# Kernel optimization log

Hardware: AMD Instinct MI355X
Metric: run time of the kernel (lower is better)

## Reference

```python
import jax, jax.numpy as jnp
import numpy as np

B, T, I, H, L, O = 512, 512, 64, 256, 3, 1  # batch, seq_len, input, hidden, layers, output


def setup_inputs() -> dict:
    key = jax.random.key(0)
    ks = jax.random.split(key, 16)
    s = 1.0 / np.sqrt(H)  # PyTorch nn.RNN init: U(-1/sqrt(H), 1/sqrt(H))
    u = lambda k, shape: jax.random.uniform(k, shape, jnp.float32, -s, s)
    inp = {"x": jax.random.normal(ks[0], (B, T, I), jnp.float32)}
    in_sizes = [I, H, H]
    for l in range(L):
        inp[f"w_ih{l}"] = u(ks[1 + 4 * l], (H, in_sizes[l]))
        inp[f"w_hh{l}"] = u(ks[2 + 4 * l], (H, H))
        inp[f"b_ih{l}"] = u(ks[3 + 4 * l], (H,))
        inp[f"b_hh{l}"] = u(ks[4 + 4 * l], (H,))
    inp["w_fc"] = u(ks[13], (O, H))
    inp["b_fc"] = u(ks[14], (O,))
    return inp


def _rnn_layer(x, w_ih, w_hh, b_ih, b_hh):
    # x: [B, T, in] -> outputs [B, T, H]; h_t = tanh(x_t W_ih^T + b_ih + h_{t-1} W_hh^T + b_hh)
    pre = jnp.einsum('bti,hi->bth', x, w_ih) + b_ih + b_hh  # input projection for all t at once

    def step(h, p_t):
        h = jnp.tanh(p_t + h @ w_hh.T)
        return h, h

    h0 = jnp.zeros((x.shape[0], w_hh.shape[0]), x.dtype)
    _, ys = jax.lax.scan(step, h0, pre.transpose(1, 0, 2))  # scan over time
    return ys.transpose(1, 0, 2)


def reference(x, w_ih0, w_hh0, b_ih0, b_hh0, w_ih1, w_hh1, b_ih1, b_hh1,
              w_ih2, w_hh2, b_ih2, b_hh2, w_fc, b_fc):
    h = _rnn_layer(x, w_ih0, w_hh0, b_ih0, b_hh0)
    h = _rnn_layer(h, w_ih1, w_hh1, b_ih1, b_hh1)
    h = _rnn_layer(h, w_ih2, w_hh2, b_ih2, b_hh2)
    out = h[:, -1, :] @ w_fc.T + b_fc  # [B, 1]
    return out.squeeze()  # [B]
```

## Files before the change

kernel.cpp:

```cpp
#include <hip/hip_runtime.h>
#include <cstdint>
#include <cstddef>

#define Tsz 512
#define TC  32
#define NCH 16

typedef _Float16 f16;
typedef _Float16 half8_t __attribute__((ext_vector_type(8)));
typedef _Float16 half4_t __attribute__((ext_vector_type(4)));
typedef float float4_t __attribute__((ext_vector_type(4)));

__device__ __forceinline__ float fast_exp2(float x) {
  float r; asm("v_exp_f32 %0, %1" : "=v"(r) : "v"(x)); return r;
}
__device__ __forceinline__ void pin(half8_t& v) { asm("" : "+v"(v)); }

#define BARRIER_LG asm volatile("s_waitcnt lgkmcnt(0)\n\ts_barrier" ::: "memory")

__device__ __forceinline__ size_t poff(int tile, int slot, int t, int j, int q) {
  return (((size_t)((tile * 2 + slot) * TC + t) * 256 + j) << 6) + ((size_t)q << 4);
}

template<int LAYER>
__device__ __forceinline__ void rec01_body(
    char* const smem, const int chunk, const int tile,
    const float* __restrict__ Pin, float* __restrict__ Pout,
    const f16* __restrict__ whh_h, const f16* __restrict__ wihn_h,
    const float* __restrict__ biasc, f16* __restrict__ st)
{
  char* const h_lds = smem;
  const int tid  = threadIdx.x;
  const int lane = tid & 63;
  const int wave = tid >> 6;
  const int m    = lane & 15;
  const int q    = lane >> 4;
  const int lo   = m * 16;
  const int slot = chunk & 1;
  const int j    = wave * 16 + m;

  half8_t whh[8], wihn[8];
  float biasn = biasc[(LAYER + 1) * 256 + j];
#pragma unroll
  for (int c = 0; c < 8; ++c) whh[c]  = *(const half8_t*)(whh_h  + j * 256 + c * 32 + q * 8);
#pragma unroll
  for (int c = 0; c < 8; ++c) wihn[c] = *(const half8_t*)(wihn_h + j * 256 + c * 32 + q * 8);
#pragma unroll
  for (int c = 0; c < 8; ++c) { pin(whh[c]); pin(wihn[c]); }

  if (tid < 512) {
    if (chunk == 0)
      *(float4_t*)(h_lds + tid * 16) = float4_t{0.f, 0.f, 0.f, 0.f};
    else
      *(float4_t*)(h_lds + tid * 16) = *(const float4_t*)((const char*)st + tile * 8192 + tid * 16);
  }

  float4_t pld[2];
  auto pload = [&](int tl, float4_t* d) {
    const int tn = (tl > TC - 1) ? (TC - 1) : tl;
    d[0] = *(const float4_t*)((const char*)Pin + poff(tile, slot, tn, j, q));
  };
  pload(0, &pld[0]); pload(1, &pld[1]);
  BARRIER_LG;

#pragma unroll 2
  for (int tl = 0; tl < TC; ++tl) {
    char* cur = h_lds + (tl & 1) * 8192;
    char* nxt = h_lds + ((tl + 1) & 1) * 8192;

    half8_t hf[4];
#pragma unroll
    for (int c = 0; c < 4; ++c) hf[c] = *(const half8_t*)(cur + (c * 4 + q) * 256 + lo);
    float4_t a0 = pld[tl & 1];
#pragma unroll
    for (int c = 0; c < 4; ++c)
      a0 = __builtin_amdgcn_mfma_f32_16x16x32_f16(hf[c], whh[c], a0, 0, 0, 0);
    float4_t b0 = {biasn, biasn, biasn, biasn};
    if (tl >= 1) {
#pragma unroll
      for (int c = 0; c < 4; ++c)
        b0 = __builtin_amdgcn_mfma_f32_16x16x32_f16(hf[c], wihn[c], b0, 0, 0, 0);
    }
#pragma unroll
    for (int c = 0; c < 4; ++c) hf[c] = *(const half8_t*)(cur + ((c + 4) * 4 + q) * 256 + lo);
    float4_t a1 = {0.f, 0.f, 0.f, 0.f};
#pragma unroll
    for (int c = 0; c < 4; ++c)
      a1 = __builtin_amdgcn_mfma_f32_16x16x32_f16(hf[c], whh[c + 4], a1, 0, 0, 0);
    if (tl >= 1) {
#pragma unroll
      for (int c = 0; c < 4; ++c)
        b0 = __builtin_amdgcn_mfma_f32_16x16x32_f16(hf[c], wihn[c + 4], b0, 0, 0, 0);
      *(float4_t*)((char*)Pout + poff(tile, slot, tl - 1, j, q)) = b0;
    }
    pload(tl + 2, &pld[tl & 1]);

    const float4_t acc = a0 + a1;
#pragma unroll
    for (int r = 0; r < 4; ++r) {
      const float e  = fast_exp2(acc[r] * 2.8853900817779268f);
      const float hv = 1.0f - 2.0f * __builtin_amdgcn_rcpf(1.0f + e);
      const int b = q * 4 + r;
      *(f16*)(nxt + (j >> 3) * 256 + b * 16 + (j & 7) * 2) = (f16)hv;
    }
    BARRIER_LG;
  }

  {
    half8_t hf[4];
    float4_t b0 = {biasn, biasn, biasn, biasn};
#pragma unroll
    for (int c = 0; c < 4; ++c) hf[c] = *(const half8_t*)(h_lds + (c * 4 + q) * 256 + lo);
#pragma unroll
    for (int c = 0; c < 4; ++c)
      b0 = __builtin_amdgcn_mfma_f32_16x16x32_f16(hf[c], wihn[c], b0, 0, 0, 0);
#pragma unroll
    for (int c = 0; c < 4; ++c) hf[c] = *(const half8_t*)(h_lds + ((c + 4) * 4 + q) * 256 + lo);
#pragma unroll
    for (int c = 0; c < 4; ++c)
      b0 = __builtin_amdgcn_mfma_f32_16x16x32_f16(hf[c], wihn[c + 4], b0, 0, 0, 0);
    *(float4_t*)((char*)Pout + poff(tile, slot, TC - 1, j, q)) = b0;
  }
  if (tid < 512)
    *(float4_t*)((char*)st + tile * 8192 + tid * 16) = *(const float4_t*)(h_lds + tid * 16);
}

template<bool REC, bool PRE>
__device__ __forceinline__ void l2_body(
    char* const smem, const int chunk, const int pre_chunk, const int tile,
    const f16* __restrict__ xh, const float* __restrict__ Pin, float* __restrict__ Pout,
    const f16* __restrict__ whh_h, const f16* __restrict__ wih0_h,
    const float* __restrict__ biasc, f16* __restrict__ st)
{
  char* const h_lds = smem;
  const int tid  = threadIdx.x;
  const int lane = tid & 63;
  const int wave = tid >> 6;
  const int m    = lane & 15;
  const int q    = lane >> 4;
  const int lo   = m * 16;
  const int slot  = chunk & 1;
  const int pslot = pre_chunk & 1;
  const int j    = wave * 16 + m;

  half8_t whh[8], wih0[2];
  float bias0 = 0.f;
  if constexpr (PRE) {
    bias0 = biasc[j];
#pragma unroll
    for (int c = 0; c < 2; ++c) wih0[c] = *(const half8_t*)(wih0_h + j * 64 + c * 32 + q * 8);
    pin(wih0[0]); pin(wih0[1]);
  }
  if constexpr (REC) {
#pragma unroll
    for (int c = 0; c < 8; ++c) whh[c] = *(const half8_t*)(whh_h + j * 256 + c * 32 + q * 8);
#pragma unroll
    for (int c = 0; c < 8; ++c) pin(whh[c]);
  }

  float4_t pld[2];
  auto pload = [&](int tl, float4_t* d) {
    const int tn = (tl > TC - 1) ? (TC - 1) : tl;
    d[0] = *(const float4_t*)((const char*)Pin + poff(tile, slot, tn, j, q));
  };
  half8_t xp[2][2];
  auto xload = [&](int tl, half8_t* d) {
    const int tn = (tl > TC - 1) ? (TC - 1) : tl;
    const f16* base = xh + ((size_t)(tile * 16 + m) * Tsz + (pre_chunk * TC + tn)) * 64 + q * 8;
    d[0] = *(const half8_t*)base;
    d[1] = *(const half8_t*)(base + 32);
  };

  if constexpr (REC) {
    if (tid < 512) {
      if (chunk == 0)
        *(float4_t*)(h_lds + tid * 16) = float4_t{0.f, 0.f, 0.f, 0.f};
      else
        *(float4_t*)(h_lds + tid * 16) = *(const float4_t*)((const char*)st + tile * 8192 + tid * 16);
    }
    pload(0, &pld[0]); pload(1, &pld[1]);
  }
  if constexpr (PRE) { xload(0, xp[0]); xload(1, xp[1]); }
  if constexpr (REC) BARRIER_LG;

#pragma unroll 2
  for (int tl = 0; tl < TC; ++tl) {
    if constexpr (REC) {
      char* cur = h_lds + (tl & 1) * 8192;
      char* nxt = h_lds + ((tl + 1) & 1) * 8192;
      half8_t hf[4];
#pragma unroll
      for (int c = 0; c < 4; ++c) hf[c] = *(const half8_t*)(cur + (c * 4 + q) * 256 + lo);
      float4_t a0 = pld[tl & 1];
#pragma unroll
      for (int c = 0; c < 4; ++c)
        a0 = __builtin_amdgcn_mfma_f32_16x16x32_f16(hf[c], whh[c], a0, 0, 0, 0);
#pragma unroll
      for (int c = 0; c < 4; ++c) hf[c] = *(const half8_t*)(cur + ((c + 4) * 4 + q) * 256 + lo);
      float4_t a1 = {0.f, 0.f, 0.f, 0.f};
#pragma unroll
      for (int c = 0; c < 4; ++c)
        a1 = __builtin_amdgcn_mfma_f32_16x16x32_f16(hf[c], whh[c + 4], a1, 0, 0, 0);
      pload(tl + 2, &pld[tl & 1]);
      const float4_t acc = a0 + a1;
#pragma unroll
      for (int r = 0; r < 4; ++r) {
        const float e  = fast_exp2(acc[r] * 2.8853900817779268f);
        const float hv = 1.0f - 2.0f * __builtin_amdgcn_rcpf(1.0f + e);
        const int b = q * 4 + r;
        *(f16*)(nxt + (j >> 3) * 256 + b * 16 + (j & 7) * 2) = (f16)hv;
      }
    }
    if constexpr (PRE) {
      float4_t b = {bias0, bias0, bias0, bias0};
      b = __builtin_amdgcn_mfma_f32_16x16x32_f16(xp[tl & 1][0], wih0[0], b, 0, 0, 0);
      b = __builtin_amdgcn_mfma_f32_16x16x32_f16(xp[tl & 1][1], wih0[1], b, 0, 0, 0);
      xload(tl + 2, xp[tl & 1]);
      *(float4_t*)((char*)Pout + poff(tile, pslot, tl, j, q)) = b;
    }
    if constexpr (REC) BARRIER_LG;
  }

  if constexpr (REC) {
    if (tid < 512)
      *(float4_t*)((char*)st + tile * 8192 + tid * 16) = *(const float4_t*)(h_lds + tid * 16);
  }
}

__global__ __launch_bounds__(1024)
void rnn_chunk_kernel(const f16* __restrict__ xh,
                      float* P0, float* P1, float* P2,
                      const f16* __restrict__ whh0h, const f16* __restrict__ whh1h,
                      const f16* __restrict__ whh2h, const f16* __restrict__ wih0h,
                      const f16* __restrict__ wih1h, const f16* __restrict__ wih2h,
                      const float* __restrict__ biasc,
                      f16* st0, f16* st1, f16* st2, int k)
{
  __shared__ __align__(16) char smem[16384];
  const int layer = blockIdx.x >> 5;
  const int tile  = blockIdx.x & 31;
  if (layer == 0) {
    if (k < NCH) rec01_body<0>(smem, k, tile, P0, P1, whh0h, wih1h, biasc, st0);
  } else if (layer == 1) {
    const int c = k - 1;
    if (c >= 0 && c < NCH) rec01_body<1>(smem, c, tile, P1, P2, whh1h, wih2h, biasc, st1);
  } else {
    const int c  = k - 2;
    const int pc = k + 1;
    const bool rec = (c >= 0 && c < NCH);
    const bool pre = (pc < NCH);
    if (rec && pre)  l2_body<true,  true >(smem, c, pc, tile, xh, P2, P0, whh2h, wih0h, biasc, st2);
    else if (rec)    l2_body<true,  false>(smem, c, pc, tile, xh, P2, P0, whh2h, wih0h, biasc, st2);
    else if (pre)    l2_body<false, true >(smem, c, pc, tile, xh, P2, P0, whh2h, wih0h, biasc, st2);
  }
}

__global__ __launch_bounds__(1024)
void pre0_kernel(const f16* __restrict__ xh, float* P0,
                 const f16* __restrict__ wih0h, const float* __restrict__ biasc)
{
  __shared__ __align__(16) char smem[16384];
  l2_body<false, true>(smem, 0, 0, blockIdx.x, xh, nullptr, P0, nullptr, wih0h, biasc, nullptr);
}

__global__ void prep_x_kernel(const float* __restrict__ x, f16* __restrict__ xh) {
  const size_t i = ((size_t)blockIdx.x * 256 + threadIdx.x) * 8;
  const float4_t v0 = *(const float4_t*)(x + i);
  const float4_t v1 = *(const float4_t*)(x + i + 4);
  half8_t o;
#pragma unroll
  for (int u = 0; u < 4; ++u) { o[u] = (f16)v0[u]; o[u + 4] = (f16)v1[u]; }
  *(half8_t*)(xh + i) = o;
}

__global__ void prep_kernel(const float* __restrict__ wih0, const float* __restrict__ whh0,
                            const float* __restrict__ bih0, const float* __restrict__ bhh0,
                            const float* __restrict__ wih1, const float* __restrict__ whh1,
                            const float* __restrict__ bih1, const float* __restrict__ bhh1,
                            const float* __restrict__ wih2, const float* __restrict__ whh2,
                            const float* __restrict__ bih2, const float* __restrict__ bhh2,
                            f16* wih0h, f16* whh0h, f16* wih1h, f16* whh1h,
                            f16* wih2h, f16* whh2h, float* biasc)
{
  const int i = blockIdx.x * 256 + threadIdx.x;
  if      (i < 16384)  wih0h[i]          = (f16)wih0[i];
  else if (i < 81920)  whh0h[i - 16384]  = (f16)whh0[i - 16384];
  else if (i < 147456) wih1h[i - 81920]  = (f16)wih1[i - 81920];
  else if (i < 212992) whh1h[i - 147456] = (f16)whh1[i - 147456];
  else if (i < 278528) wih2h[i - 212992] = (f16)wih2[i - 212992];
  else if (i < 344064) whh2h[i - 278528] = (f16)whh2[i - 278528];
  else if (i < 344320) biasc[i - 344064]       = bih0[i - 344064] + bhh0[i - 344064];
  else if (i < 344576) biasc[256 + i - 344320] = bih1[i - 344320] + bhh1[i - 344320];
  else if (i < 344832) biasc[512 + i - 344576] = bih2[i - 344576] + bhh2[i - 344576];
}

__global__ void fc_kernel(const f16* __restrict__ st2, const float* __restrict__ w_fc,
                          const float* __restrict__ b_fc, float* __restrict__ outp) {
  const int b = blockIdx.x;
  const int lane = threadIdx.x;
  const int tile = b >> 4, bl = b & 15;
  const int j = lane * 4;
  const char* hp = (const char*)st2 + tile * 8192 + (j >> 3) * 256 + bl * 16 + (j & 7) * 2;
  const half4_t hv = *(const half4_t*)hp;
  const float4_t w = *(const float4_t*)(w_fc + j);
  float s = (float)hv[0] * w[0] + (float)hv[1] * w[1] + (float)hv[2] * w[2] + (float)hv[3] * w[3];
#pragma unroll
  for (int off = 32; off > 0; off >>= 1) s += __shfl_down(s, off, 64);
  if (lane == 0) outp[b] = s + b_fc[0];
}

extern "C" void kernel_launch(void* const* d_in, const int* in_sizes, int n_in,
                              void* d_out, int out_size, void* d_ws, size_t ws_size,
                              hipStream_t stream) {
  const float* x     = (const float*)d_in[0];
  const float* w_ih0 = (const float*)d_in[1];
  const float* w_hh0 = (const float*)d_in[2];
  const float* b_ih0 = (const float*)d_in[3];
  const float* b_hh0 = (const float*)d_in[4];
  const float* w_ih1 = (const float*)d_in[5];
  const float* w_hh1 = (const float*)d_in[6];
  const float* b_ih1 = (const float*)d_in[7];
  const float* b_hh1 = (const float*)d_in[8];
  const float* w_ih2 = (const float*)d_in[9];
  const float* w_hh2 = (const float*)d_in[10];
  const float* b_ih2 = (const float*)d_in[11];
  const float* b_hh2 = (const float*)d_in[12];
  const float* w_fc  = (const float*)d_in[13];
  const float* b_fc  = (const float*)d_in[14];

  char* ws = (char*)d_ws;
  float* P0   = (float*)(ws);
  float* P1   = (float*)(ws + 33554432);
  float* P2   = (float*)(ws + 67108864);
  f16* st0    = (f16*)(ws + 100663296);
  f16* st1    = (f16*)(ws + 100925440);
  f16* st2    = (f16*)(ws + 101187584);
  f16* wih0h  = (f16*)(ws + 101449728);
  f16* whh0h  = (f16*)(ws + 101482496);
  f16* wih1h  = (f16*)(ws + 101613568);
  f16* whh1h  = (f16*)(ws + 101744640);
  f16* wih2h  = (f16*)(ws + 101875712);
  f16* whh2h  = (f16*)(ws + 102006784);
  float* biasc = (float*)(ws + 102137856);
  f16* xh     = (f16*)(ws + 102141952);

  prep_x_kernel<<<8192, 256, 0, stream>>>(x, xh);
  prep_kernel<<<1347, 256, 0, stream>>>(w_ih0, w_hh0, b_ih0, b_hh0,
                                        w_ih1, w_hh1, b_ih1, b_hh1,
                                        w_ih2, w_hh2, b_ih2, b_hh2,
                                        wih0h, whh0h, wih1h, whh1h, wih2h, whh2h, biasc);
  pre0_kernel<<<32, 1024, 0, stream>>>(xh, P0, wih0h, biasc);
  for (int k = 0; k < NCH + 2; ++k)
    rnn_chunk_kernel<<<96, 1024, 0, stream>>>(xh, P0, P1, P2,
                                              whh0h, whh1h, whh2h,
                                              wih0h, wih1h, wih2h,
                                              biasc, st0, st1, st2, k);
  fc_kernel<<<512, 64, 0, stream>>>(st2, w_fc, b_fc, (float*)d_out);
}
```

Baseline: 954.0 us.

## Defer next-layer input projection by one step and interleave MFMA chains

In the layer-0/1 recurrence, the next layer's input projection now uses the hidden state from the previous step, kept in registers, instead of the current one. This takes it off the critical path between the h load and the tanh, and it is interleaved as two independent accumulator chains. All eight h fragments are loaded at once, the P prefetch is issued earlier, and the two whh MFMA chains are interleaved so they overlap. Layer 2 moves its x-projection work inside the recurrent branch to overlap with it. The cost is a larger register footprint (double-buffered hf arrays), which may add pressure at 1024 threads, plus an extra epilogue step.

```diff
diff --git a/kernel.cpp b/kernel.cpp
--- a/kernel.cpp
+++ b/kernel.cpp
@@ -22,12 +22,11 @@
   return (((size_t)((tile * 2 + slot) * TC + t) * 256 + j) << 6) + ((size_t)q << 4);
 }
 
-template<int LAYER>
 __device__ __forceinline__ void rec01_body(
     char* const smem, const int chunk, const int tile,
     const float* __restrict__ Pin, float* __restrict__ Pout,
     const f16* __restrict__ whh_h, const f16* __restrict__ wihn_h,
-    const float* __restrict__ biasc, f16* __restrict__ st)
+    const float* __restrict__ bias_n, f16* __restrict__ st)
 {
   char* const h_lds = smem;
   const int tid  = threadIdx.x;
@@ -40,7 +39,7 @@
   const int j    = wave * 16 + m;
 
   half8_t whh[8], wihn[8];
-  float biasn = biasc[(LAYER + 1) * 256 + j];
+  const float biasn = bias_n[j];
 #pragma unroll
   for (int c = 0; c < 8; ++c) whh[c]  = *(const half8_t*)(whh_h  + j * 256 + c * 32 + q * 8);
 #pragma unroll
@@ -61,41 +60,41 @@
     d[0] = *(const float4_t*)((const char*)Pin + poff(tile, slot, tn, j, q));
   };
   pload(0, &pld[0]); pload(1, &pld[1]);
+
+  half8_t hf[2][8];
   BARRIER_LG;
 
 #pragma unroll 2
   for (int tl = 0; tl < TC; ++tl) {
-    char* cur = h_lds + (tl & 1) * 8192;
-    char* nxt = h_lds + ((tl + 1) & 1) * 8192;
-
-    half8_t hf[4];
-#pragma unroll
-    for (int c = 0; c < 4; ++c) hf[c] = *(const half8_t*)(cur + (c * 4 + q) * 256 + lo);
-    float4_t a0 = pld[tl & 1];
-#pragma unroll
-    for (int c = 0; c < 4; ++c)
-      a0 = __builtin_amdgcn_mfma_f32_16x16x32_f16(hf[c], whh[c], a0, 0, 0, 0);
-    float4_t b0 = {biasn, biasn, biasn, biasn};
-    if (tl >= 1) {
-#pragma unroll
-      for (int c = 0; c < 4; ++c)
-        b0 = __builtin_amdgcn_mfma_f32_16x16x32_f16(hf[c], wihn[c], b0, 0, 0, 0);
-    }
-#pragma unroll
-    for (int c = 0; c < 4; ++c) hf[c] = *(const half8_t*)(cur + ((c + 4) * 4 + q) * 256 + lo);
+    const int cu = tl & 1, pv = cu ^ 1;
+    char* cur = h_lds + cu * 8192;
+    char* nxt = h_lds + pv * 8192;
+
+#pragma unroll
+    for (int c = 0; c < 8; ++c) hf[cu][c] = *(const half8_t*)(cur + (c * 4 + q) * 256 + lo);
+
+    float4_t a0 = pld[cu];
+    pload(tl + 2, &pld[cu]);
+
+    if (tl >= 2) {
+      float4_t b0 = {biasn, biasn, biasn, biasn};
+      float4_t b1 = {0.f, 0.f, 0.f, 0.f};
+#pragma unroll
+      for (int c = 0; c < 4; ++c) {
+        b0 = __builtin_amdgcn_mfma_f32_16x16x32_f16(hf[pv][c],     wihn[c],     b0, 0, 0, 0);
+        b1 = __builtin_amdgcn_mfma_f32_16x16x32_f16(hf[pv][c + 4], wihn[c + 4], b1, 0, 0, 0);
+      }
+      *(float4_t*)((char*)Pout + poff(tile, slot, tl - 2, j, q)) = b0 + b1;
+    }
+
     float4_t a1 = {0.f, 0.f, 0.f, 0.f};
 #pragma unroll
-    for (int c = 0; c < 4; ++c)
-      a1 = __builtin_amdgcn_mfma_f32_16x16x32_f16(hf[c], whh[c + 4], a1, 0, 0, 0);
-    if (tl >= 1) {
-#pragma unroll
-      for (int c = 0; c < 4; ++c)
-        b0 = __builtin_amdgcn_mfma_f32_16x16x32_f16(hf[c], wihn[c + 4], b0, 0, 0, 0);
-      *(float4_t*)((char*)Pout + poff(tile, slot, tl - 1, j, q)) = b0;
-    }
-    pload(tl + 2, &pld[tl & 1]);
-
+    for (int c = 0; c < 4; ++c) {
+      a0 = __builtin_amdgcn_mfma_f32_16x16x32_f16(hf[cu][c],     whh[c],     a0, 0, 0, 0);
+      a1 = __builtin_amdgcn_mfma_f32_16x16x32_f16(hf[cu][c + 4], whh[c + 4], a1, 0, 0, 0);
+    }
     const float4_t acc = a0 + a1;
+
 #pragma unroll
     for (int r = 0; r < 4; ++r) {
       const float e  = fast_exp2(acc[r] * 2.8853900817779268f);
@@ -107,19 +106,27 @@
   }
 
   {
-    half8_t hf[4];
     float4_t b0 = {biasn, biasn, biasn, biasn};
-#pragma unroll
-    for (int c = 0; c < 4; ++c) hf[c] = *(const half8_t*)(h_lds + (c * 4 + q) * 256 + lo);
-#pragma unroll
-    for (int c = 0; c < 4; ++c)
-      b0 = __builtin_amdgcn_mfma_f32_16x16x32_f16(hf[c], wihn[c], b0, 0, 0, 0);
-#pragma unroll
-    for (int c = 0; c < 4; ++c) hf[c] = *(const half8_t*)(h_lds + ((c + 4) * 4 + q) * 256 + lo);
-#pragma unroll
-    for (int c = 0; c < 4; ++c)
-      b0 = __builtin_amdgcn_mfma_f32_16x16x32_f16(hf[c], wihn[c + 4], b0, 0, 0, 0);
-    *(float4_t*)((char*)Pout + poff(tile, slot, TC - 1, j, q)) = b0;
+    float4_t b1 = {0.f, 0.f, 0.f, 0.f};
+#pragma unroll
+    for (int c = 0; c < 4; ++c) {
+      b0 = __builtin_amdgcn_mfma_f32_16x16x32_f16(hf[1][c],     wihn[c],     b0, 0, 0, 0);
+      b1 = __builtin_amdgcn_mfma_f32_16x16x32_f16(hf[1][c + 4], wihn[c + 4], b1, 0, 0, 0);
+    }
+    *(float4_t*)((char*)Pout + poff(tile, slot, TC - 2, j, q)) = b0 + b1;
+  }
+  {
+    half8_t hx[8];
+#pragma unroll
+    for (int c = 0; c < 8; ++c) hx[c] = *(const half8_t*)(h_lds + (c * 4 + q) * 256 + lo);
+    float4_t b0 = {biasn, biasn, biasn, biasn};
+    float4_t b1 = {0.f, 0.f, 0.f, 0.f};
+#pragma unroll
+    for (int c = 0; c < 4; ++c) {
+      b0 = __builtin_amdgcn_mfma_f32_16x16x32_f16(hx[c],     wihn[c],     b0, 0, 0, 0);
+      b1 = __builtin_amdgcn_mfma_f32_16x16x32_f16(hx[c + 4], wihn[c + 4], b1, 0, 0, 0);
+    }
+    *(float4_t*)((char*)Pout + poff(tile, slot, TC - 1, j, q)) = b0 + b1;
   }
   if (tid < 512)
     *(float4_t*)((char*)st + tile * 8192 + tid * 16) = *(const float4_t*)(h_lds + tid * 16);
@@ -185,23 +192,28 @@
 
 #pragma unroll 2
   for (int tl = 0; tl < TC; ++tl) {
+    const int cu = tl & 1;
     if constexpr (REC) {
-      char* cur = h_lds + (tl & 1) * 8192;
-      char* nxt = h_lds + ((tl + 1) & 1) * 8192;
-      half8_t hf[4];
-#pragma unroll
-      for (int c = 0; c < 4; ++c) hf[c] = *(const half8_t*)(cur + (c * 4 + q) * 256 + lo);
-      float4_t a0 = pld[tl & 1];
-#pragma unroll
-      for (int c = 0; c < 4; ++c)
-        a0 = __builtin_amdgcn_mfma_f32_16x16x32_f16(hf[c], whh[c], a0, 0, 0, 0);
-#pragma unroll
-      for (int c = 0; c < 4; ++c) hf[c] = *(const half8_t*)(cur + ((c + 4) * 4 + q) * 256 + lo);
+      char* cur = h_lds + cu * 8192;
+      char* nxt = h_lds + (cu ^ 1) * 8192;
+      half8_t hf[8];
+#pragma unroll
+      for (int c = 0; c < 8; ++c) hf[c] = *(const half8_t*)(cur + (c * 4 + q) * 256 + lo);
+      float4_t a0 = pld[cu];
+      pload(tl + 2, &pld[cu]);
+      if constexpr (PRE) {
+        float4_t b = {bias0, bias0, bias0, bias0};
+        b = __builtin_amdgcn_mfma_f32_16x16x32_f16(xp[cu][0], wih0[0], b, 0, 0, 0);
+        b = __builtin_amdgcn_mfma_f32_16x16x32_f16(xp[cu][1], wih0[1], b, 0, 0, 0);
+        xload(tl + 2, xp[cu]);
+        *(float4_t*)((char*)Pout + poff(tile, pslot, tl, j, q)) = b;
+      }
       float4_t a1 = {0.f, 0.f, 0.f, 0.f};
 #pragma unroll
-      for (int c = 0; c < 4; ++c)
-        a1 = __builtin_amdgcn_mfma_f32_16x16x32_f16(hf[c], whh[c + 4], a1, 0, 0, 0);
-      pload(tl + 2, &pld[tl & 1]);
+      for (int c = 0; c < 4; ++c) {
+        a0 = __builtin_amdgcn_mfma_f32_16x16x32_f16(hf[c],     whh[c],     a0, 0, 0, 0);
+        a1 = __builtin_amdgcn_mfma_f32_16x16x32_f16(hf[c + 4], whh[c + 4], a1, 0, 0, 0);
+      }
       const float4_t acc = a0 + a1;
 #pragma unroll
       for (int r = 0; r < 4; ++r) {
@@ -210,12 +222,11 @@
         const int b = q * 4 + r;
         *(f16*)(nxt + (j >> 3) * 256 + b * 16 + (j & 7) * 2) = (f16)hv;
       }
-    }
-    if constexpr (PRE) {
+    } else if constexpr (PRE) {
       float4_t b = {bias0, bias0, bias0, bias0};
-      b = __builtin_amdgcn_mfma_f32_16x16x32_f16(xp[tl & 1][0], wih0[0], b, 0, 0, 0);
-      b = __builtin_amdgcn_mfma_f32_16x16x32_f16(xp[tl & 1][1], wih0[1], b, 0, 0, 0);
-      xload(tl + 2, xp[tl & 1]);
+      b = __builtin_amdgcn_mfma_f32_16x16x32_f16(xp[cu][0], wih0[0], b, 0, 0, 0);
+      b = __builtin_amdgcn_mfma_f32_16x16x32_f16(xp[cu][1], wih0[1], b, 0, 0, 0);
+      xload(tl + 2, xp[cu]);
       *(float4_t*)((char*)Pout + poff(tile, pslot, tl, j, q)) = b;
     }
     if constexpr (REC) BARRIER_LG;
@@ -240,10 +251,10 @@
   const int layer = blockIdx.x >> 5;
   const int tile  = blockIdx.x & 31;
   if (layer == 0) {
-    if (k < NCH) rec01_body<0>(smem, k, tile, P0, P1, whh0h, wih1h, biasc, st0);
+    if (k < NCH) rec01_body(smem, k, tile, P0, P1, whh0h, wih1h, biasc + 256, st0);
   } else if (layer == 1) {
     const int c = k - 1;
-    if (c >= 0 && c < NCH) rec01_body<1>(smem, c, tile, P1, P2, whh1h, wih2h, biasc, st1);
+    if (c >= 0 && c < NCH) rec01_body(smem, c, tile, P1, P2, whh1h, wih2h, biasc + 512, st1);
   } else {
     const int c  = k - 2;
     const int pc = k + 1;
```

Measured after the change: 2.526 ms. +164.8%, slower.

## Transpose MFMA operands and pad hidden-state LDS rows for vectorized stores

Applied to the files above, without the earlier changes.

Swaps the A/B operands of the recurrent MFMAs so each lane produces four consecutive hidden units for one batch row. The hidden state in LDS becomes row-major per batch with rows padded to 528 bytes, and each lane writes one half4 instead of four scattered f16 stores. P buffers, bias loads, the state save/restore and the FC read are re-laid out to match. The goal is fewer LDS store instructions and fewer bank conflicts on the per-step critical path, at the cost of slightly larger state buffers.

```diff
diff --git a/kernel.cpp b/kernel.cpp
--- a/kernel.cpp
+++ b/kernel.cpp
@@ -5,6 +5,8 @@
 #define Tsz 512
 #define TC  32
 #define NCH 16
+#define IMG  8448
+#define STSZ 8448
 
 typedef _Float16 f16;
 typedef _Float16 half8_t __attribute__((ext_vector_type(8)));
@@ -18,16 +20,15 @@
 
 #define BARRIER_LG asm volatile("s_waitcnt lgkmcnt(0)\n\ts_barrier" ::: "memory")
 
-__device__ __forceinline__ size_t poff(int tile, int slot, int t, int j, int q) {
-  return (((size_t)((tile * 2 + slot) * TC + t) * 256 + j) << 6) + ((size_t)q << 4);
-}
-
-template<int LAYER>
+__device__ __forceinline__ size_t pbase(int tile, int slot, int t) {
+  return ((size_t)((tile * 2 + slot) * TC + t)) << 14;
+}
+
 __device__ __forceinline__ void rec01_body(
     char* const smem, const int chunk, const int tile,
     const float* __restrict__ Pin, float* __restrict__ Pout,
     const f16* __restrict__ whh_h, const f16* __restrict__ wihn_h,
-    const float* __restrict__ biasc, f16* __restrict__ st)
+    const float* __restrict__ bias_n, f16* __restrict__ st)
 {
   char* const h_lds = smem;
   const int tid  = threadIdx.x;
@@ -35,94 +36,94 @@
   const int wave = tid >> 6;
   const int m    = lane & 15;
   const int q    = lane >> 4;
-  const int lo   = m * 16;
-  const int slot = chunk & 1;
-  const int j    = wave * 16 + m;
+  const int jb   = wave * 16 + q * 4;
+  const int rb   = m * 528 + q * 16;
 
   half8_t whh[8], wihn[8];
-  float biasn = biasc[(LAYER + 1) * 256 + j];
-#pragma unroll
-  for (int c = 0; c < 8; ++c) whh[c]  = *(const half8_t*)(whh_h  + j * 256 + c * 32 + q * 8);
-#pragma unroll
-  for (int c = 0; c < 8; ++c) wihn[c] = *(const half8_t*)(wihn_h + j * 256 + c * 32 + q * 8);
+  const float4_t biasn = *(const float4_t*)(bias_n + jb);
+#pragma unroll
+  for (int c = 0; c < 8; ++c) whh[c]  = *(const half8_t*)(whh_h  + (wave * 16 + m) * 256 + c * 32 + q * 8);
+#pragma unroll
+  for (int c = 0; c < 8; ++c) wihn[c] = *(const half8_t*)(wihn_h + (wave * 16 + m) * 256 + c * 32 + q * 8);
 #pragma unroll
   for (int c = 0; c < 8; ++c) { pin(whh[c]); pin(wihn[c]); }
 
-  if (tid < 512) {
+  if (tid < 528) {
     if (chunk == 0)
       *(float4_t*)(h_lds + tid * 16) = float4_t{0.f, 0.f, 0.f, 0.f};
     else
-      *(float4_t*)(h_lds + tid * 16) = *(const float4_t*)((const char*)st + tile * 8192 + tid * 16);
-  }
-
+      *(float4_t*)(h_lds + tid * 16) = *(const float4_t*)((const char*)st + tile * STSZ + tid * 16);
+  }
+
+  const int slot = chunk & 1;
   float4_t pld[2];
   auto pload = [&](int tl, float4_t* d) {
     const int tn = (tl > TC - 1) ? (TC - 1) : tl;
-    d[0] = *(const float4_t*)((const char*)Pin + poff(tile, slot, tn, j, q));
+    d[0] = *(const float4_t*)((const char*)Pin + pbase(tile, slot, tn) + (m << 10) + (jb << 2));
   };
   pload(0, &pld[0]); pload(1, &pld[1]);
   BARRIER_LG;
 
 #pragma unroll 2
   for (int tl = 0; tl < TC; ++tl) {
-    char* cur = h_lds + (tl & 1) * 8192;
-    char* nxt = h_lds + ((tl + 1) & 1) * 8192;
+    char* cur = h_lds + (tl & 1) * IMG;
+    char* nxt = h_lds + ((tl + 1) & 1) * IMG;
 
     half8_t hf[4];
 #pragma unroll
-    for (int c = 0; c < 4; ++c) hf[c] = *(const half8_t*)(cur + (c * 4 + q) * 256 + lo);
+    for (int c = 0; c < 4; ++c) hf[c] = *(const half8_t*)(cur + rb + c * 64);
     float4_t a0 = pld[tl & 1];
 #pragma unroll
     for (int c = 0; c < 4; ++c)
-      a0 = __builtin_amdgcn_mfma_f32_16x16x32_f16(hf[c], whh[c], a0, 0, 0, 0);
-    float4_t b0 = {biasn, biasn, biasn, biasn};
+      a0 = __builtin_amdgcn_mfma_f32_16x16x32_f16(whh[c], hf[c], a0, 0, 0, 0);
+    float4_t b0 = biasn;
     if (tl >= 1) {
 #pragma unroll
       for (int c = 0; c < 4; ++c)
-        b0 = __builtin_amdgcn_mfma_f32_16x16x32_f16(hf[c], wihn[c], b0, 0, 0, 0);
-    }
-#pragma unroll
-    for (int c = 0; c < 4; ++c) hf[c] = *(const half8_t*)(cur + ((c + 4) * 4 + q) * 256 + lo);
+        b0 = __builtin_amdgcn_mfma_f32_16x16x32_f16(wihn[c], hf[c], b0, 0, 0, 0);
+    }
+#pragma unroll
+    for (int c = 0; c < 4; ++c) hf[c] = *(const half8_t*)(cur + rb + (c + 4) * 64);
     float4_t a1 = {0.f, 0.f, 0.f, 0.f};
 #pragma unroll
     for (int c = 0; c < 4; ++c)
-      a1 = __builtin_amdgcn_mfma_f32_16x16x32_f16(hf[c], whh[c + 4], a1, 0, 0, 0);
+      a1 = __builtin_amdgcn_mfma_f32_16x16x32_f16(whh[c + 4], hf[c], a1, 0, 0, 0);
     if (tl >= 1) {
 #pragma unroll
       for (int c = 0; c < 4; ++c)
-        b0 = __builtin_amdgcn_mfma_f32_16x16x32_f16(hf[c], wihn[c + 4], b0, 0, 0, 0);
-      *(float4_t*)((char*)Pout + poff(tile, slot, tl - 1, j, q)) = b0;
+        b0 = __builtin_amdgcn_mfma_f32_16x16x32_f16(wihn[c + 4], hf[c], b0, 0, 0, 0);
+      *(float4_t*)((char*)Pout + pbase(tile, slot, tl - 1) + (m << 10) + (jb << 2)) = b0;
     }
     pload(tl + 2, &pld[tl & 1]);
 
     const float4_t acc = a0 + a1;
+    half4_t hv4;
 #pragma unroll
     for (int r = 0; r < 4; ++r) {
       const float e  = fast_exp2(acc[r] * 2.8853900817779268f);
-      const float hv = 1.0f - 2.0f * __builtin_amdgcn_rcpf(1.0f + e);
-      const int b = q * 4 + r;
-      *(f16*)(nxt + (j >> 3) * 256 + b * 16 + (j & 7) * 2) = (f16)hv;
-    }
+      hv4[r] = (f16)(1.0f - 2.0f * __builtin_amdgcn_rcpf(1.0f + e));
+    }
+    *(half4_t*)(nxt + m * 528 + jb * 2) = hv4;
     BARRIER_LG;
   }
 
   {
     half8_t hf[4];
-    float4_t b0 = {biasn, biasn, biasn, biasn};
-#pragma unroll
-    for (int c = 0; c < 4; ++c) hf[c] = *(const half8_t*)(h_lds + (c * 4 + q) * 256 + lo);
+    float4_t b0 = biasn;
+#pragma unroll
+    for (int c = 0; c < 4; ++c) hf[c] = *(const half8_t*)(h_lds + rb + c * 64);
 #pragma unroll
     for (int c = 0; c < 4; ++c)
-      b0 = __builtin_amdgcn_mfma_f32_16x16x32_f16(hf[c], wihn[c], b0, 0, 0, 0);
-#pragma unroll
-    for (int c = 0; c < 4; ++c) hf[c] = *(const half8_t*)(h_lds + ((c + 4) * 4 + q) * 256 + lo);
+      b0 = __builtin_amdgcn_mfma_f32_16x16x32_f16(wihn[c], hf[c], b0, 0, 0, 0);
+#pragma unroll
+    for (int c = 0; c < 4; ++c) hf[c] = *(const half8_t*)(h_lds + rb + (c + 4) * 64);
 #pragma unroll
     for (int c = 0; c < 4; ++c)
-      b0 = __builtin_amdgcn_mfma_f32_16x16x32_f16(hf[c], wihn[c + 4], b0, 0, 0, 0);
-    *(float4_t*)((char*)Pout + poff(tile, slot, TC - 1, j, q)) = b0;
-  }
-  if (tid < 512)
-    *(float4_t*)((char*)st + tile * 8192 + tid * 16) = *(const float4_t*)(h_lds + tid * 16);
+      b0 = __builtin_amdgcn_mfma_f32_16x16x32_f16(wihn[c + 4], hf[c], b0, 0, 0, 0);
+    *(float4_t*)((char*)Pout + pbase(tile, slot, TC - 1) + (m << 10) + (jb << 2)) = b0;
+  }
+  if (tid < 528)
+    *(float4_t*)((char*)st + tile * STSZ + tid * 16) = *(const float4_t*)(h_lds + tid * 16);
 }
 
 template<bool REC, bool PRE>
@@ -138,22 +139,22 @@
   const int wave = tid >> 6;
   const int m    = lane & 15;
   const int q    = lane >> 4;
-  const int lo   = m * 16;
+  const int jb   = wave * 16 + q * 4;
+  const int rb   = m * 528 + q * 16;
   const int slot  = chunk & 1;
   const int pslot = pre_chunk & 1;
-  const int j    = wave * 16 + m;
 
   half8_t whh[8], wih0[2];
-  float bias0 = 0.f;
+  float4_t bias0 = {0.f, 0.f, 0.f, 0.f};
   if constexpr (PRE) {
-    bias0 = biasc[j];
-#pragma unroll
-    for (int c = 0; c < 2; ++c) wih0[c] = *(const half8_t*)(wih0_h + j * 64 + c * 32 + q * 8);
+    bias0 = *(const float4_t*)(biasc + jb);
+#pragma unroll
+    for (int c = 0; c < 2; ++c) wih0[c] = *(const half8_t*)(wih0_h + (wave * 16 + m) * 64 + c * 32 + q * 8);
     pin(wih0[0]); pin(wih0[1]);
   }
   if constexpr (REC) {
 #pragma unroll
-    for (int c = 0; c < 8; ++c) whh[c] = *(const half8_t*)(whh_h + j * 256 + c * 32 + q * 8);
+    for (int c = 0; c < 8; ++c) whh[c] = *(const half8_t*)(whh_h + (wave * 16 + m) * 256 + c * 32 + q * 8);
 #pragma unroll
     for (int c = 0; c < 8; ++c) pin(whh[c]);
   }
@@ -161,7 +162,7 @@
   float4_t pld[2];
   auto pload = [&](int tl, float4_t* d) {
     const int tn = (tl > TC - 1) ? (TC - 1) : tl;
-    d[0] = *(const float4_t*)((const char*)Pin + poff(tile, slot, tn, j, q));
+    d[0] = *(const float4_t*)((const char*)Pin + pbase(tile, slot, tn) + (m << 10) + (jb << 2));
   };
   half8_t xp[2][2];
   auto xload = [&](int tl, half8_t* d) {
@@ -172,11 +173,11 @@
   };
 
   if constexpr (REC) {
-    if (tid < 512) {
+    if (tid < 528) {
       if (chunk == 0)
         *(float4_t*)(h_lds + tid * 16) = float4_t{0.f, 0.f, 0.f, 0.f};
       else
-        *(float4_t*)(h_lds + tid * 16) = *(const float4_t*)((const char*)st + tile * 8192 + tid * 16);
+        *(float4_t*)(h_lds + tid * 16) = *(const float4_t*)((const char*)st + tile * STSZ + tid * 16);
     }
     pload(0, &pld[0]); pload(1, &pld[1]);
   }
@@ -185,45 +186,46 @@
 
 #pragma unroll 2
   for (int tl = 0; tl < TC; ++tl) {
+    const int cu = tl & 1;
     if constexpr (REC) {
-      char* cur = h_lds + (tl & 1) * 8192;
-      char* nxt = h_lds + ((tl + 1) & 1) * 8192;
+      char* cur = h_lds + cu * IMG;
+      char* nxt = h_lds + (cu ^ 1) * IMG;
       half8_t hf[4];
 #pragma unroll
-      for (int c = 0; c < 4; ++c) hf[c] = *(const half8_t*)(cur + (c * 4 + q) * 256 + lo);
-      float4_t a0 = pld[tl & 1];
+      for (int c = 0; c < 4; ++c) hf[c] = *(const half8_t*)(cur + rb + c * 64);
+      float4_t a0 = pld[cu];
 #pragma unroll
       for (int c = 0; c < 4; ++c)
-        a0 = __builtin_amdgcn_mfma_f32_16x16x32_f16(hf[c], whh[c], a0, 0, 0, 0);
-#pragma unroll
-      for (int c = 0; c < 4; ++c) hf[c] = *(const half8_t*)(cur + ((c + 4) * 4 + q) * 256 + lo);
+        a0 = __builtin_amdgcn_mfma_f32_16x16x32_f16(whh[c], hf[c], a0, 0, 0, 0);
+#pragma unroll
+      for (int c = 0; c < 4; ++c) hf[c] = *(const half8_t*)(cur + rb + (c + 4) * 64);
       float4_t a1 = {0.f, 0.f, 0.f, 0.f};
 #pragma unroll
       for (int c = 0; c < 4; ++c)
-        a1 = __builtin_amdgcn_mfma_f32_16x16x32_f16(hf[c], whh[c + 4], a1, 0, 0, 0);
-      pload(tl + 2, &pld[tl & 1]);
+        a1 = __builtin_amdgcn_mfma_f32_16x16x32_f16(whh[c + 4], hf[c], a1, 0, 0, 0);
+      pload(tl + 2, &pld[cu]);
       const float4_t acc = a0 + a1;
+      half4_t hv4;
 #pragma unroll
       for (int r = 0; r < 4; ++r) {
         const float e  = fast_exp2(acc[r] * 2.8853900817779268f);
-        const float hv = 1.0f - 2.0f * __builtin_amdgcn_rcpf(1.0f + e);
-        const int b = q * 4 + r;
-        *(f16*)(nxt + (j >> 3) * 256 + b * 16 + (j & 7) * 2) = (f16)hv;
+        hv4[r] = (f16)(1.0f - 2.0f * __builtin_amdgcn_rcpf(1.0f + e));
       }
+      *(half4_t*)(nxt + m * 528 + jb * 2) = hv4;
     }
     if constexpr (PRE) {
-      float4_t b = {bias0, bias0, bias0, bias0};
-      b = __builtin_amdgcn_mfma_f32_16x16x32_f16(xp[tl & 1][0], wih0[0], b, 0, 0, 0);
-      b = __builtin_amdgcn_mfma_f32_16x16x32_f16(xp[tl & 1][1], wih0[1], b, 0, 0, 0);
-      xload(tl + 2, xp[tl & 1]);
-      *(float4_t*)((char*)Pout + poff(tile, pslot, tl, j, q)) = b;
+      float4_t b = bias0;
+      b = __builtin_amdgcn_mfma_f32_16x16x32_f16(wih0[0], xp[cu][0], b, 0, 0, 0);
+      b = __builtin_amdgcn_mfma_f32_16x16x32_f16(wih0[1], xp[cu][1], b, 0, 0, 0);
+      xload(tl + 2, xp[cu]);
+      *(float4_t*)((char*)Pout + pbase(tile, pslot, tl) + (m << 10) + (jb << 2)) = b;
     }
     if constexpr (REC) BARRIER_LG;
   }
 
   if constexpr (REC) {
-    if (tid < 512)
-      *(float4_t*)((char*)st + tile * 8192 + tid * 16) = *(const float4_t*)(h_lds + tid * 16);
+    if (tid < 528)
+      *(float4_t*)((char*)st + tile * STSZ + tid * 16) = *(const float4_t*)(h_lds + tid * 16);
   }
 }
 
@@ -236,14 +238,14 @@
                       const float* __restrict__ biasc,
                       f16* st0, f16* st1, f16* st2, int k)
 {
-  __shared__ __align__(16) char smem[16384];
+  __shared__ __align__(16) char smem[2 * IMG];
   const int layer = blockIdx.x >> 5;
   const int tile  = blockIdx.x & 31;
   if (layer == 0) {
-    if (k < NCH) rec01_body<0>(smem, k, tile, P0, P1, whh0h, wih1h, biasc, st0);
+    if (k < NCH) rec01_body(smem, k, tile, P0, P1, whh0h, wih1h, biasc + 256, st0);
   } else if (layer == 1) {
     const int c = k - 1;
-    if (c >= 0 && c < NCH) rec01_body<1>(smem, c, tile, P1, P2, whh1h, wih2h, biasc, st1);
+    if (c >= 0 && c < NCH) rec01_body(smem, c, tile, P1, P2, whh1h, wih2h, biasc + 512, st1);
   } else {
     const int c  = k - 2;
     const int pc = k + 1;
@@ -259,7 +261,7 @@
 void pre0_kernel(const f16* __restrict__ xh, float* P0,
                  const f16* __restrict__ wih0h, const float* __restrict__ biasc)
 {
-  __shared__ __align__(16) char smem[16384];
+  __shared__ __align__(16) char smem[2 * IMG];
   l2_body<false, true>(smem, 0, 0, blockIdx.x, xh, nullptr, P0, nullptr, wih0h, biasc, nullptr);
 }
 
@@ -300,8 +302,7 @@
   const int lane = threadIdx.x;
   const int tile = b >> 4, bl = b & 15;
   const int j = lane * 4;
-  const char* hp = (const char*)st2 + tile * 8192 + (j >> 3) * 256 + bl * 16 + (j & 7) * 2;
-  const half4_t hv = *(const half4_t*)hp;
+  const half4_t hv = *(const half4_t*)((const char*)st2 + tile * STSZ + bl * 528 + j * 2);
   const float4_t w = *(const float4_t*)(w_fc + j);
   float s = (float)hv[0] * w[0] + (float)hv[1] * w[1] + (float)hv[2] * w[2] + (float)hv[3] * w[3];
 #pragma unroll
@@ -333,16 +334,16 @@
   float* P1   = (float*)(ws + 33554432);
   float* P2   = (float*)(ws + 67108864);
   f16* st0    = (f16*)(ws + 100663296);
-  f16* st1    = (f16*)(ws + 100925440);
-  f16* st2    = (f16*)(ws + 101187584);
-  f16* wih0h  = (f16*)(ws + 101449728);
-  f16* whh0h  = (f16*)(ws + 101482496);
-  f16* wih1h  = (f16*)(ws + 101613568);
-  f16* whh1h  = (f16*)(ws + 101744640);
-  f16* wih2h  = (f16*)(ws + 101875712);
-  f16* whh2h  = (f16*)(ws + 102006784);
-  float* biasc = (float*)(ws + 102137856);
-  f16* xh     = (f16*)(ws + 102141952);
+  f16* st1    = (f16*)(ws + 101187584);
+  f16* st2    = (f16*)(ws + 101711872);
+  f16* wih0h  = (f16*)(ws + 102236160);
+  f16* whh0h  = (f16*)(ws + 102268928);
+  f16* wih1h  = (f16*)(ws + 102400000);
+  f16* whh1h  = (f16*)(ws + 102531072);
+  f16* wih2h  = (f16*)(ws + 102662144);
+  f16* whh2h  = (f16*)(ws + 102793216);
+  float* biasc = (float*)(ws + 102924288);
+  f16* xh     = (f16*)(ws + 102928384);
 
   prep_x_kernel<<<8192, 256, 0, stream>>>(x, xh);
   prep_kernel<<<1347, 256, 0, stream>>>(w_ih0, w_hh0, b_ih0, b_hh0,
```

After: 1.063 ms. 11.4% more time.
